# Optimization experiments

Measured on AMD Instinct MI355X. Metric: run time of the kernel, lower is better.

Reference implementation:

```python
import jax, jax.numpy as jnp
import numpy as np

D_MODEL = 512
HEADS = 8
FF_HIDDEN = 1024
EPS = 1e-6


def setup_inputs() -> dict:
    key = jax.random.key(0)
    ks = jax.random.split(key, 12)
    s = 1.0 / np.sqrt(D_MODEL)
    inp = {
        'x': jax.random.normal(ks[0], (2, 4096, D_MODEL), dtype=jnp.float32),
        'Wq': jax.random.normal(ks[1], (D_MODEL, D_MODEL), dtype=jnp.float32) * s,
        'bq': jnp.zeros((D_MODEL,), jnp.float32),
        'Wk': jax.random.normal(ks[2], (D_MODEL, D_MODEL), dtype=jnp.float32) * s,
        'bk': jnp.zeros((D_MODEL,), jnp.float32),
        'Wv': jax.random.normal(ks[3], (D_MODEL, D_MODEL), dtype=jnp.float32) * s,
        'bv': jnp.zeros((D_MODEL,), jnp.float32),
        'Wo': jax.random.normal(ks[4], (D_MODEL, D_MODEL), dtype=jnp.float32) * s,
        'bo': jnp.zeros((D_MODEL,), jnp.float32),
        'a1': jnp.ones((D_MODEL,), jnp.float32),
        'b1': jnp.zeros((D_MODEL,), jnp.float32),
        'a2': jnp.ones((D_MODEL,), jnp.float32),
        'b2': jnp.zeros((D_MODEL,), jnp.float32),
        'W1': jax.random.normal(ks[5], (D_MODEL, FF_HIDDEN), dtype=jnp.float32) * s,
        'c1': jnp.zeros((FF_HIDDEN,), jnp.float32),
        'W2': jax.random.normal(ks[6], (FF_HIDDEN, D_MODEL), dtype=jnp.float32) * (1.0 / np.sqrt(FF_HIDDEN)),
        'c2': jnp.zeros((D_MODEL,), jnp.float32),
    }
    return inp


def _layer_norm(x, a, b):
    # Faithful to source: uses unbiased std (torch default) and divides by (std + eps)
    mean = jnp.mean(x, axis=-1, keepdims=True)
    std = jnp.std(x, axis=-1, keepdims=True, ddof=1)
    return a * ((x - mean) / (std + EPS)) + b


def _encoder_block(x, Wq, bq, Wk, bk, Wv, bv, Wo, bo, a1, b1, a2, b2, W1, c1, W2, c2):
    B, S, D = x.shape
    H, dk = HEADS, D // HEADS
    q = (x @ Wq + bq).reshape(B, S, H, dk).transpose(0, 2, 1, 3)  # [B,H,S,dk]
    k = (x @ Wk + bk).reshape(B, S, H, dk).transpose(0, 2, 1, 3)
    v = (x @ Wv + bv).reshape(B, S, H, dk).transpose(0, 2, 1, 3)
    scores = jnp.einsum('bhqd,bhkd->bhqk', q, k) / np.sqrt(dk)
    probs = jax.nn.softmax(scores, axis=-1)
    attn = jnp.einsum('bhqk,bhkd->bhqd', probs, v)
    concat = attn.transpose(0, 2, 1, 3).reshape(B, S, D)
    attn_out = concat @ Wo + bo
    x = _layer_norm(x + attn_out, a1, b1)  # dropout = identity (eval mode)
    ffn = jax.nn.relu(x @ W1 + c1) @ W2 + c2
    return _layer_norm(x + ffn, a2, b2)


def reference(x, Wq, bq, Wk, bk, Wv, bv, Wo, bo, a1, b1, a2, b2, W1, c1, W2, c2):
    return _encoder_block(x, Wq, bq, Wk, bk, Wv, bv, Wo, bo, a1, b1, a2, b2, W1, c1, W2, c2)
```

## Files before the change

kernel.cpp:

```cpp
#include <hip/hip_runtime.h>
#include <stdint.h>

typedef short short8 __attribute__((ext_vector_type(8)));
typedef float f32x4 __attribute__((ext_vector_type(4)));
typedef float f32x16 __attribute__((ext_vector_type(16)));
typedef unsigned int u32x4 __attribute__((ext_vector_type(4)));

#define LOG2E 1.44269504088896f

__device__ __forceinline__ unsigned short f2b(float f) {
  union { float f; unsigned int u; } x; x.f = f;
  unsigned int u = x.u;
  unsigned int r = (u + 0x7fffu + ((u >> 16) & 1u)) >> 16;
  return (unsigned short)r;
}
__device__ __forceinline__ float b2f(unsigned short s) {
  union { unsigned int u; float f; } x; x.u = ((unsigned int)s) << 16;
  return x.f;
}
__device__ __forceinline__ void gl16(const void* g, void* l) {
  __builtin_amdgcn_global_load_lds((const __attribute__((address_space(1))) void*)g,
                                   (__attribute__((address_space(3))) void*)l, 16, 0, 0);
}
__device__ __forceinline__ unsigned int cvtpk(float lo, float hi) {
  unsigned int r;
  asm("v_cvt_pk_bf16_f32 %0, %1, %2" : "=v"(r) : "v"(lo), "v"(hi));
  return r;
}
__device__ __forceinline__ void plswap(unsigned int& a, unsigned int& b) {
  asm volatile("v_permlane32_swap_b32 %0, %1" : "+v"(a), "+v"(b));
}

__global__ __launch_bounds__(256) void castx_k(const float* __restrict__ X,
                                               unsigned short* __restrict__ Xb) {
  int i = blockIdx.x * 256 + threadIdx.x;
  const float* p = X + (size_t)i * 8;
  float4 a = *(const float4*)(p);
  float4 b = *(const float4*)(p + 4);
  short8 o;
  o[0] = (short)f2b(a.x); o[1] = (short)f2b(a.y);
  o[2] = (short)f2b(a.z); o[3] = (short)f2b(a.w);
  o[4] = (short)f2b(b.x); o[5] = (short)f2b(b.y);
  o[6] = (short)f2b(b.z); o[7] = (short)f2b(b.w);
  *(short8*)(Xb + (size_t)i * 8) = o;
}

__global__ __launch_bounds__(256) void catb_k(const float* __restrict__ bq,
                                              const float* __restrict__ bk,
                                              const float* __restrict__ bv,
                                              float* __restrict__ Bqkv) {
  for (int i = threadIdx.x; i < 1536; i += 256) {
    float v = (i < 512) ? bq[i] : (i < 1024 ? bk[i - 512] : bv[i - 1024]);
    Bqkv[i] = v;
  }
}

__global__ __launch_bounds__(256) void wtrans_k(const float* __restrict__ W,
                                                unsigned short* __restrict__ WT,
                                                int K, int N) {
  __shared__ float t[64][65];
  int k0 = blockIdx.x * 64, n0 = blockIdx.y * 64;
  for (int i = threadIdx.x; i < 4096; i += 256) {
    int r = i >> 6, c = i & 63;
    t[r][c] = W[(size_t)(k0 + r) * N + n0 + c];
  }
  __syncthreads();
  for (int i = threadIdx.x; i < 4096; i += 256) {
    int r = i >> 6, c = i & 63;
    WT[(size_t)(n0 + r) * K + k0 + c] = f2b(t[c][r]);
  }
}

__global__ __launch_bounds__(256) void vtrans_k(const unsigned short* __restrict__ V,
                                                unsigned short* __restrict__ Vt) {
  __shared__ unsigned short t[64][65];
  int s0 = blockIdx.x * 64;
  int bh = blockIdx.y;
  int b = bh >> 3, h = bh & 7;
  for (int i = threadIdx.x; i < 4096; i += 256) {
    int r = i >> 6, c = i & 63;
    t[r][c] = V[(size_t)(b * 4096 + s0 + r) * 512 + h * 64 + c];
  }
  __syncthreads();
  for (int i = threadIdx.x; i < 4096; i += 256) {
    int r = i >> 6, c = i & 63;
    Vt[(size_t)(bh * 64 + r) * 4096 + s0 + c] = t[c][r];
  }
}

template <int EPI>
__global__ __launch_bounds__(256) void gemm_bt(
    const unsigned short* __restrict__ A, const unsigned short* __restrict__ BT,
    const float* __restrict__ bias, float* __restrict__ Cf,
    unsigned short* __restrict__ Cb, int M, int N, int K) {
  __shared__ unsigned short As[128 * 32];
  __shared__ unsigned short Bs[128 * 32];
  int t = threadIdx.x, w = t >> 6, l = t & 63;
  int bm = blockIdx.x, bn = blockIdx.y;
  int wm = w >> 1, wn = w & 1;
  int g = l >> 4, ln = l & 15;
  f32x4 acc[4][4] = {};
  const unsigned short* Arow = A + (size_t)bm * 128 * K;
  const unsigned short* Brow = BT + (size_t)bn * 128 * K;
  int nk = K >> 5;
  for (int kt = 0; kt < nk; ++kt) {
    int k0 = kt * 32;
#pragma unroll
    for (int i = 0; i < 2; ++i) {
      int cl = i * 256 + t;
      int r = cl >> 2, c = cl & 3;
      char* ldsA = (char*)As + (size_t)(i * 256 + w * 64) * 16;
      char* ldsB = (char*)Bs + (size_t)(i * 256 + w * 64) * 16;
      gl16(Arow + (size_t)r * K + k0 + c * 8, ldsA);
      gl16(Brow + (size_t)r * K + k0 + c * 8, ldsB);
    }
    __syncthreads();
    short8 af[4], bf[4];
    int ko = g * 8;
#pragma unroll
    for (int i = 0; i < 4; ++i)
      af[i] = *(const short8*)&As[(wm * 64 + i * 16 + ln) * 32 + ko];
#pragma unroll
    for (int j = 0; j < 4; ++j)
      bf[j] = *(const short8*)&Bs[(wn * 64 + j * 16 + ln) * 32 + ko];
    __builtin_amdgcn_s_setprio(1);
#pragma unroll
    for (int i = 0; i < 4; ++i)
#pragma unroll
      for (int j = 0; j < 4; ++j)
        acc[i][j] = __builtin_amdgcn_mfma_f32_16x16x32_bf16(af[i], bf[j], acc[i][j], 0, 0, 0);
    __builtin_amdgcn_s_setprio(0);
    __syncthreads();
  }
#pragma unroll
  for (int i = 0; i < 4; ++i) {
    int row = bm * 128 + wm * 64 + i * 16 + g * 4;
#pragma unroll
    for (int j = 0; j < 4; ++j) {
      int col = bn * 128 + wn * 64 + j * 16 + ln;
      float bv = bias[col];
#pragma unroll
      for (int r = 0; r < 4; ++r) {
        float v = acc[i][j][r] + bv;
        if constexpr (EPI == 2) v = v > 0.f ? v : 0.f;
        if constexpr (EPI == 0) Cf[(size_t)(row + r) * N + col] = v;
        else if constexpr (EPI == 3)
          Cb[(size_t)(col >> 9) * 4194304 + (size_t)(row + r) * 512 + (col & 511)] = f2b(v);
        else Cb[(size_t)(row + r) * N + col] = f2b(v);
      }
    }
  }
}

__global__ __launch_bounds__(256) void gemm64_k(
    const unsigned short* __restrict__ A, const unsigned short* __restrict__ BT,
    const float* __restrict__ bias, float* __restrict__ Cf, int M, int N, int K) {
  __shared__ unsigned short As[64 * 32];
  __shared__ unsigned short Bs[128 * 32];
  int t = threadIdx.x, w = t >> 6, l = t & 63;
  int bm = blockIdx.x, bn = blockIdx.y;
  int wm = w >> 1, wn = w & 1;
  int g = l >> 4, ln = l & 15;
  f32x4 acc[2][4] = {};
  const unsigned short* Arow = A + (size_t)bm * 64 * K;
  const unsigned short* Brow = BT + (size_t)bn * 128 * K;
  int nk = K >> 5;
  for (int kt = 0; kt < nk; ++kt) {
    int k0 = kt * 32;
    {
      int r = t >> 2, c = t & 3;
      gl16(Arow + (size_t)r * K + k0 + c * 8, (char*)As + (size_t)(w * 64) * 16);
    }
#pragma unroll
    for (int i = 0; i < 2; ++i) {
      int cl = i * 256 + t;
      int r = cl >> 2, c = cl & 3;
      char* ldsB = (char*)Bs + (size_t)(i * 256 + w * 64) * 16;
      gl16(Brow + (size_t)r * K + k0 + c * 8, ldsB);
    }
    __syncthreads();
    short8 af[2], bf[4];
    int ko = g * 8;
#pragma unroll
    for (int i = 0; i < 2; ++i)
      af[i] = *(const short8*)&As[(wm * 32 + i * 16 + ln) * 32 + ko];
#pragma unroll
    for (int j = 0; j < 4; ++j)
      bf[j] = *(const short8*)&Bs[(wn * 64 + j * 16 + ln) * 32 + ko];
    __builtin_amdgcn_s_setprio(1);
#pragma unroll
    for (int i = 0; i < 2; ++i)
#pragma unroll
      for (int j = 0; j < 4; ++j)
        acc[i][j] = __builtin_amdgcn_mfma_f32_16x16x32_bf16(af[i], bf[j], acc[i][j], 0, 0, 0);
    __builtin_amdgcn_s_setprio(0);
    __syncthreads();
  }
#pragma unroll
  for (int i = 0; i < 2; ++i) {
    int row = bm * 64 + wm * 32 + i * 16 + g * 4;
#pragma unroll
    for (int j = 0; j < 4; ++j) {
      int col = bn * 128 + wn * 64 + j * 16 + ln;
      float bv = bias[col];
#pragma unroll
      for (int r = 0; r < 4; ++r)
        Cf[(size_t)(row + r) * N + col] = acc[i][j][r] + bv;
    }
  }
}

__global__ __launch_bounds__(256, 2) void attn_k(
    const unsigned short* __restrict__ Q, const unsigned short* __restrict__ Kb,
    const unsigned short* __restrict__ Vt, float* __restrict__ Opart,
    float* __restrict__ L) {
  __shared__ unsigned short Ks[2][4096];
  __shared__ unsigned short Vs[3][4096];
  int tid = threadIdx.x, wv = tid >> 6, lane = tid & 63;
  int l31 = lane & 31, hi = lane >> 5;
  int qb = blockIdx.x, bh = blockIdx.y, z = blockIdx.z;
  int b = bh >> 3, h = bh & 7;
  int q0 = qb * 256 + wv * 64;
  int kvbase = z * 2048;

  short8 qfA[4], qfB[4];
  {
    const float QSC = 0.125f * LOG2E;
    const unsigned short* qpA = Q + (size_t)(b * 4096 + q0 + l31) * 512 + h * 64;
    const unsigned short* qpB = qpA + 32 * 512;
#pragma unroll
    for (int ks = 0; ks < 4; ++ks) {
      short8 va = *(const short8*)(qpA + ks * 16 + hi * 8);
      short8 vb = *(const short8*)(qpB + ks * 16 + hi * 8);
#pragma unroll
      for (int j = 0; j < 8; ++j) {
        va[j] = (short)f2b(b2f((unsigned short)va[j]) * QSC);
        vb[j] = (short)f2b(b2f((unsigned short)vb[j]) * QSC);
      }
      qfA[ks] = va; qfB[ks] = vb;
    }
  }

  short8 ones;
#pragma unroll
  for (int j = 0; j < 8; ++j) ones[j] = (short)0x3F80;

  f32x16 oA0 = {}, oA1 = {}, oB0 = {}, oB1 = {}, laccA = {}, laccB = {};

  int skk[2], sc[2];
#pragma unroll
  for (int i = 0; i < 2; ++i) {
    int u = i * 256 + tid;
    int r2 = u >> 4, s = u & 15;
    skk[i] = 2 * r2 + (s & 1);
    sc[i] = ((s >> 1) ^ (r2 & 7)) * 8;
  }

  auto stage = [&](char* kb_lds, char* vb_lds, int kv) {
    const unsigned short* ksrc = Kb + (size_t)(b * 4096 + kv) * 512 + h * 64;
    const unsigned short* vsrc = Vt + (size_t)(bh * 64) * 4096 + kv;
#pragma unroll
    for (int i = 0; i < 2; ++i) {
      gl16(ksrc + (size_t)skk[i] * 512 + sc[i], kb_lds + (size_t)(i * 256 + wv * 64) * 16);
      gl16(vsrc + (size_t)skk[i] * 4096 + sc[i], vb_lds + (size_t)(i * 256 + wv * 64) * 16);
    }
  };

  int r2a = l31 >> 1, par = l31 & 1, perm = r2a & 7;
  int rdb = r2a * 256 + (par << 4);

  auto qk = [&](const char* kbase, f32x16& sA0, f32x16& sA1, f32x16& sB0, f32x16& sB1) {
    __builtin_amdgcn_s_setprio(1);
#pragma unroll
    for (int ks = 0; ks < 4; ++ks) {
      int c16 = ks * 2 + hi;
      int byteA = rdb + (((c16 ^ perm) << 1) << 4);
      short8 k0 = *(const short8*)(kbase + byteA);
      short8 k1 = *(const short8*)(kbase + byteA + 4096);
      sA0 = __builtin_amdgcn_mfma_f32_32x32x16_bf16(k0, qfA[ks], sA0, 0, 0, 0);
      sA1 = __builtin_amdgcn_mfma_f32_32x32x16_bf16(k1, qfA[ks], sA1, 0, 0, 0);
      sB0 = __builtin_amdgcn_mfma_f32_32x32x16_bf16(k0, qfB[ks], sB0, 0, 0, 0);
      sB1 = __builtin_amdgcn_mfma_f32_32x32x16_bf16(k1, qfB[ks], sB1, 0, 0, 0);
    }
    __builtin_amdgcn_s_setprio(0);
  };

  auto pv = [&](const char* vbase, const short8* pfA, const short8* pfB) {
    __builtin_amdgcn_s_setprio(1);
#pragma unroll
    for (int ks = 0; ks < 4; ++ks) {
      int c16 = ks * 2 + hi;
      int byteA = rdb + (((c16 ^ perm) << 1) << 4);
      short8 v0 = *(const short8*)(vbase + byteA);
      short8 v1 = *(const short8*)(vbase + byteA + 4096);
      oA0 = __builtin_amdgcn_mfma_f32_32x32x16_bf16(v0, pfA[ks], oA0, 0, 0, 0);
      oA1 = __builtin_amdgcn_mfma_f32_32x32x16_bf16(v1, pfA[ks], oA1, 0, 0, 0);
      oB0 = __builtin_amdgcn_mfma_f32_32x32x16_bf16(v0, pfB[ks], oB0, 0, 0, 0);
      oB1 = __builtin_amdgcn_mfma_f32_32x32x16_bf16(v1, pfB[ks], oB1, 0, 0, 0);
      laccA = __builtin_amdgcn_mfma_f32_32x32x16_bf16(ones, pfA[ks], laccA, 0, 0, 0);
      laccB = __builtin_amdgcn_mfma_f32_32x32x16_bf16(ones, pfB[ks], laccB, 0, 0, 0);
    }
    __builtin_amdgcn_s_setprio(0);
  };

  auto exppack = [&](f32x16& s0, f32x16& s1, short8* pf) {
#pragma unroll
    for (int r = 0; r < 16; ++r) s0[r] = __builtin_amdgcn_exp2f(s0[r]);
#pragma unroll
    for (int r = 0; r < 16; ++r) s1[r] = __builtin_amdgcn_exp2f(s1[r]);
    unsigned int u0 = cvtpk(s0[0], s0[1]), u1 = cvtpk(s0[4], s0[5]);
    plswap(u0, u1);
    unsigned int u2 = cvtpk(s0[2], s0[3]), u3 = cvtpk(s0[6], s0[7]);
    plswap(u2, u3);
    unsigned int u4 = cvtpk(s0[8], s0[9]), u5 = cvtpk(s0[12], s0[13]);
    plswap(u4, u5);
    unsigned int u6 = cvtpk(s0[10], s0[11]), u7 = cvtpk(s0[14], s0[15]);
    plswap(u6, u7);
    union { u32x4 u; short8 s; } cv;
    cv.u = (u32x4){u0, u2, u1, u3}; pf[0] = cv.s;
    cv.u = (u32x4){u4, u6, u5, u7}; pf[1] = cv.s;
    unsigned int w0 = cvtpk(s1[0], s1[1]), w1 = cvtpk(s1[4], s1[5]);
    plswap(w0, w1);
    unsigned int w2 = cvtpk(s1[2], s1[3]), w3 = cvtpk(s1[6], s1[7]);
    plswap(w2, w3);
    unsigned int w4 = cvtpk(s1[8], s1[9]), w5 = cvtpk(s1[12], s1[13]);
    plswap(w4, w5);
    unsigned int w6 = cvtpk(s1[10], s1[11]), w7 = cvtpk(s1[14], s1[15]);
    plswap(w6, w7);
    cv.u = (u32x4){w0, w2, w1, w3}; pf[2] = cv.s;
    cv.u = (u32x4){w4, w6, w5, w7}; pf[3] = cv.s;
  };

  char* k0b = (char*)&Ks[0][0];
  char* k1b = (char*)&Ks[1][0];
  char* vA = (char*)&Vs[0][0];
  char* vB = (char*)&Vs[1][0];
  char* vC = (char*)&Vs[2][0];
  stage(k0b, vA, kvbase);
  __syncthreads();
  stage(k1b, vB, kvbase + 64);

  f32x16 sA0 = {}, sA1 = {}, sB0 = {}, sB1 = {};
  qk(k0b, sA0, sA1, sB0, sB1);
  short8 pfA[4], pfB[4];
  exppack(sA0, sA1, pfA);
  exppack(sB0, sB1, pfB);

#pragma unroll 1
  for (int t = 1; t < 32; ++t) {
    __syncthreads();
    char* kr = (t & 1) ? k1b : k0b;
    char* kw = (t & 1) ? k0b : k1b;
    if (t < 31) stage(kw, vC, kvbase + (t + 1) * 64);
    sA0 = (f32x16){}; sA1 = (f32x16){}; sB0 = (f32x16){}; sB1 = (f32x16){};
    qk(kr, sA0, sA1, sB0, sB1);
    pv(vA, pfA, pfB);
    exppack(sA0, sA1, pfA);
    exppack(sB0, sB1, pfB);
    char* tmp = vA; vA = vB; vB = vC; vC = tmp;
  }
  pv(vA, pfA, pfB);

  int plane = z * 16 + bh;
  float* op = Opart + (size_t)plane * 262144;
  int qA = q0 + l31, qB = q0 + 32 + l31;
#pragma unroll
  for (int r = 0; r < 16; ++r) {
    int dr = (r & 3) + 8 * (r >> 2) + 4 * hi;
    op[(size_t)dr * 4096 + qA] = oA0[r];
    op[(size_t)(dr + 32) * 4096 + qA] = oA1[r];
    op[(size_t)dr * 4096 + qB] = oB0[r];
    op[(size_t)(dr + 32) * 4096 + qB] = oB1[r];
  }
  if (hi == 0) {
    L[(size_t)plane * 4096 + qA] = laccA[0];
    L[(size_t)plane * 4096 + qB] = laccB[0];
  }
}

__global__ __launch_bounds__(256) void comb_k(const float* __restrict__ Opart,
                                              const float* __restrict__ L,
                                              unsigned short* __restrict__ O) {
  __shared__ float sli[64];
  __shared__ unsigned short tt[64][80];
  int tid = threadIdx.x;
  int qt = blockIdx.x, bh = blockIdx.y;
  int b = bh >> 3, h = bh & 7;
  int q0 = qt * 64;
  if (tid < 64) {
    int q = q0 + tid;
    sli[tid] = 1.0f / (L[(size_t)bh * 4096 + q] + L[(size_t)(16 + bh) * 4096 + q]);
  }
  __syncthreads();
  const float* p0 = Opart + (size_t)bh * 262144;
  const float* p1 = Opart + (size_t)(16 + bh) * 262144;
  int d = tid >> 2, qg = tid & 3;
#pragma unroll
  for (int i = 0; i < 16; ++i) {
    int qq = qg * 16 + i;
    size_t idx = (size_t)d * 4096 + q0 + qq;
    tt[qq][d] = f2b((p0[idx] + p1[idx]) * sli[qq]);
  }
  __syncthreads();
  int qr = tid >> 2, dc = tid & 3;
  short8 v0 = *(const short8*)&tt[qr][dc * 16];
  short8 v1 = *(const short8*)&tt[qr][dc * 16 + 8];
  size_t row = (size_t)(b * 4096 + q0 + qr);
  *(short8*)(O + row * 512 + h * 64 + dc * 16) = v0;
  *(short8*)(O + row * 512 + h * 64 + dc * 16 + 8) = v1;
}

template <bool WB>
__global__ __launch_bounds__(256) void ln_k(const float* __restrict__ X,
                                            const float* __restrict__ Y,
                                            const float* __restrict__ gamma,
                                            const float* __restrict__ beta,
                                            float* __restrict__ outf,
                                            unsigned short* __restrict__ outb) {
  int w = threadIdx.x >> 6, l = threadIdx.x & 63;
  size_t row = (size_t)blockIdx.x * 4 + w;
  const float* xr = X + row * 512;
  const float* yr = Y + row * 512;
  float vals[8];
  float s = 0.f, ss = 0.f;
#pragma unroll
  for (int i = 0; i < 2; ++i) {
    float4 a = *(const float4*)(xr + l * 8 + i * 4);
    float4 c = *(const float4*)(yr + l * 8 + i * 4);
    vals[i * 4 + 0] = a.x + c.x; vals[i * 4 + 1] = a.y + c.y;
    vals[i * 4 + 2] = a.z + c.z; vals[i * 4 + 3] = a.w + c.w;
  }
#pragma unroll
  for (int j = 0; j < 8; ++j) { s += vals[j]; ss += vals[j] * vals[j]; }
#pragma unroll
  for (int off = 1; off < 64; off <<= 1) { s += __shfl_xor(s, off); ss += __shfl_xor(ss, off); }
  float mean = s * (1.f / 512.f);
  float var = fmaxf((ss - 512.f * mean * mean) * (1.f / 511.f), 0.f);
  float inv = 1.f / (sqrtf(var) + 1e-6f);
  unsigned short bvals[8];
#pragma unroll
  for (int i = 0; i < 2; ++i) {
    float4 gm = *(const float4*)(gamma + l * 8 + i * 4);
    float4 bt = *(const float4*)(beta + l * 8 + i * 4);
    float4 o;
    o.x = gm.x * ((vals[i * 4 + 0] - mean) * inv) + bt.x;
    o.y = gm.y * ((vals[i * 4 + 1] - mean) * inv) + bt.y;
    o.z = gm.z * ((vals[i * 4 + 2] - mean) * inv) + bt.z;
    o.w = gm.w * ((vals[i * 4 + 3] - mean) * inv) + bt.w;
    *(float4*)(outf + row * 512 + l * 8 + i * 4) = o;
    if constexpr (WB) {
      bvals[i * 4 + 0] = f2b(o.x); bvals[i * 4 + 1] = f2b(o.y);
      bvals[i * 4 + 2] = f2b(o.z); bvals[i * 4 + 3] = f2b(o.w);
    }
  }
  if constexpr (WB) {
    short8 pk;
#pragma unroll
    for (int j = 0; j < 8; ++j) pk[j] = (short)bvals[j];
    *(short8*)(outb + row * 512 + l * 8) = pk;
  }
}

extern "C" void kernel_launch(void* const* d_in, const int* in_sizes, int n_in,
                              void* d_out, int out_size, void* d_ws, size_t ws_size,
                              hipStream_t stream) {
  const float* x  = (const float*)d_in[0];
  const float* Wq = (const float*)d_in[1];
  const float* bq = (const float*)d_in[2];
  const float* Wk = (const float*)d_in[3];
  const float* bk = (const float*)d_in[4];
  const float* Wv = (const float*)d_in[5];
  const float* bv = (const float*)d_in[6];
  const float* Wo = (const float*)d_in[7];
  const float* bo = (const float*)d_in[8];
  const float* a1 = (const float*)d_in[9];
  const float* b1 = (const float*)d_in[10];
  const float* a2 = (const float*)d_in[11];
  const float* b2 = (const float*)d_in[12];
  const float* W1 = (const float*)d_in[13];
  const float* c1 = (const float*)d_in[14];
  const float* W2 = (const float*)d_in[15];
  const float* c2 = (const float*)d_in[16];

  char* ws = (char*)d_ws;
  const size_t MB = 1024 * 1024;
  unsigned short* Xb  = (unsigned short*)(ws + 0);
  unsigned short* Qb  = (unsigned short*)(ws + 8 * MB);
  unsigned short* Kbf = (unsigned short*)(ws + 16 * MB);
  unsigned short* Vb  = (unsigned short*)(ws + 24 * MB);
  unsigned short* Vtb = (unsigned short*)(ws + 32 * MB);
  unsigned short* WqkvT = (unsigned short*)(ws + 40 * MB);
  unsigned short* WoT = (unsigned short*)(ws + 41 * MB + 512 * 1024);
  unsigned short* W1T = (unsigned short*)(ws + 42 * MB);
  unsigned short* W2T = (unsigned short*)(ws + 43 * MB);
  float* AO = (float*)(ws + 44 * MB);
  float* Y1 = (float*)(ws + 60 * MB);
  unsigned short* Att = Xb;
  unsigned short* Y1b = Qb;
  unsigned short* Hb  = Kbf;
  float* Opart = AO;
  float* L = (float*)(ws + 24 * MB);
  float* Bqkv = Y1;

  castx_k<<<2048, 256, 0, stream>>>(x, Xb);
  catb_k<<<1, 256, 0, stream>>>(bq, bk, bv, Bqkv);
  wtrans_k<<<dim3(8, 8), 256, 0, stream>>>(Wq, WqkvT, 512, 512);
  wtrans_k<<<dim3(8, 8), 256, 0, stream>>>(Wk, WqkvT + 512 * 512, 512, 512);
  wtrans_k<<<dim3(8, 8), 256, 0, stream>>>(Wv, WqkvT + 2 * 512 * 512, 512, 512);
  wtrans_k<<<dim3(8, 8), 256, 0, stream>>>(Wo, WoT, 512, 512);
  wtrans_k<<<dim3(8, 16), 256, 0, stream>>>(W1, W1T, 512, 1024);
  wtrans_k<<<dim3(16, 8), 256, 0, stream>>>(W2, W2T, 1024, 512);

  gemm_bt<3><<<dim3(64, 12), 256, 0, stream>>>(Xb, WqkvT, Bqkv, nullptr, Qb, 8192, 1536, 512);

  vtrans_k<<<dim3(64, 16), 256, 0, stream>>>(Vb, Vtb);
  attn_k<<<dim3(16, 16, 2), 256, 0, stream>>>(Qb, Kbf, Vtb, Opart, L);
  comb_k<<<dim3(64, 16), 256, 0, stream>>>(Opart, L, Att);

  gemm64_k<<<dim3(128, 4), 256, 0, stream>>>(Att, WoT, bo, AO, 8192, 512, 512);
  ln_k<true><<<2048, 256, 0, stream>>>(x, AO, a1, b1, Y1, Y1b);
  gemm_bt<2><<<dim3(64, 8), 256, 0, stream>>>(Y1b, W1T, c1, nullptr, Hb, 8192, 1024, 512);
  gemm64_k<<<dim3(128, 4), 256, 0, stream>>>(Hb, W2T, c2, AO, 8192, 512, 1024);
  ln_k<false><<<2048, 256, 0, stream>>>(Y1, AO, a2, b2, (float*)d_out, nullptr);
}
```

Baseline: 227.8 us.

## Fuse LayerNorm into GEMMs, write V transposed from QKV GEMM, fold Q scale

Several changes at once. The Wo and W2 GEMMs become a 16-row-by-512-column kernel that adds the residual and applies LayerNorm in its epilogue, which removes the fp32 AO round-trip and the separate ln_k launches. The QKV GEMM writes V straight into the transposed layout, so vtrans_k goes away, and the Q softmax scale is folded into Wq and bq. Attention partial outputs are stored as bf16 instead of fp32, and the first QK MFMA takes a zero accumulator. Risks: the new GEMM tile is narrow in M and reloads the whole B matrix per block, the bf16 partials lose precision, and the transposed V writes are strided.

```diff
diff --git a/kernel.cpp b/kernel.cpp
--- a/kernel.cpp
+++ b/kernel.cpp
@@ -2,11 +2,13 @@
 #include <stdint.h>
 
 typedef short short8 __attribute__((ext_vector_type(8)));
+typedef short short4v __attribute__((ext_vector_type(4)));
 typedef float f32x4 __attribute__((ext_vector_type(4)));
 typedef float f32x16 __attribute__((ext_vector_type(16)));
 typedef unsigned int u32x4 __attribute__((ext_vector_type(4)));
 
 #define LOG2E 1.44269504088896f
+#define QSCALE (0.125f * LOG2E)
 
 __device__ __forceinline__ unsigned short f2b(float f) {
   union { float f; unsigned int u; } x; x.f = f;
@@ -50,14 +52,14 @@
                                               const float* __restrict__ bv,
                                               float* __restrict__ Bqkv) {
   for (int i = threadIdx.x; i < 1536; i += 256) {
-    float v = (i < 512) ? bq[i] : (i < 1024 ? bk[i - 512] : bv[i - 1024]);
+    float v = (i < 512) ? bq[i] * QSCALE : (i < 1024 ? bk[i - 512] : bv[i - 1024]);
     Bqkv[i] = v;
   }
 }
 
 __global__ __launch_bounds__(256) void wtrans_k(const float* __restrict__ W,
                                                 unsigned short* __restrict__ WT,
-                                                int K, int N) {
+                                                int K, int N, float scale) {
   __shared__ float t[64][65];
   int k0 = blockIdx.x * 64, n0 = blockIdx.y * 64;
   for (int i = threadIdx.x; i < 4096; i += 256) {
@@ -67,24 +69,7 @@
   __syncthreads();
   for (int i = threadIdx.x; i < 4096; i += 256) {
     int r = i >> 6, c = i & 63;
-    WT[(size_t)(n0 + r) * K + k0 + c] = f2b(t[c][r]);
-  }
-}
-
-__global__ __launch_bounds__(256) void vtrans_k(const unsigned short* __restrict__ V,
-                                                unsigned short* __restrict__ Vt) {
-  __shared__ unsigned short t[64][65];
-  int s0 = blockIdx.x * 64;
-  int bh = blockIdx.y;
-  int b = bh >> 3, h = bh & 7;
-  for (int i = threadIdx.x; i < 4096; i += 256) {
-    int r = i >> 6, c = i & 63;
-    t[r][c] = V[(size_t)(b * 4096 + s0 + r) * 512 + h * 64 + c];
-  }
-  __syncthreads();
-  for (int i = threadIdx.x; i < 4096; i += 256) {
-    int r = i >> 6, c = i & 63;
-    Vt[(size_t)(bh * 64 + r) * 4096 + s0 + c] = t[c][r];
+    WT[(size_t)(n0 + r) * K + k0 + c] = f2b(t[c][r] * scale);
   }
 }
 
@@ -139,80 +124,130 @@
     for (int j = 0; j < 4; ++j) {
       int col = bn * 128 + wn * 64 + j * 16 + ln;
       float bv = bias[col];
+      float vv[4];
 #pragma unroll
       for (int r = 0; r < 4; ++r) {
         float v = acc[i][j][r] + bv;
         if constexpr (EPI == 2) v = v > 0.f ? v : 0.f;
-        if constexpr (EPI == 0) Cf[(size_t)(row + r) * N + col] = v;
-        else if constexpr (EPI == 3)
-          Cb[(size_t)(col >> 9) * 4194304 + (size_t)(row + r) * 512 + (col & 511)] = f2b(v);
-        else Cb[(size_t)(row + r) * N + col] = f2b(v);
+        vv[r] = v;
       }
-    }
-  }
-}
-
-__global__ __launch_bounds__(256) void gemm64_k(
+      if constexpr (EPI == 3) {
+        if (col < 1024) {
+#pragma unroll
+          for (int r = 0; r < 4; ++r)
+            Cb[(size_t)(col >> 9) * 4194304 + (size_t)(row + r) * 512 + (col & 511)] = f2b(vv[r]);
+        } else {
+          short4v pk;
+#pragma unroll
+          for (int r = 0; r < 4; ++r) pk[r] = (short)f2b(vv[r]);
+          *(short4v*)((unsigned short*)Cf +
+                      (size_t)((row >> 12) * 512 + (col & 511)) * 4096 + (row & 4095)) = pk;
+        }
+      } else {
+#pragma unroll
+        for (int r = 0; r < 4; ++r)
+          Cb[(size_t)(row + r) * N + col] = f2b(vv[r]);
+      }
+    }
+  }
+}
+
+template <bool WB>
+__global__ __launch_bounds__(512) void gemmln_k(
     const unsigned short* __restrict__ A, const unsigned short* __restrict__ BT,
-    const float* __restrict__ bias, float* __restrict__ Cf, int M, int N, int K) {
-  __shared__ unsigned short As[64 * 32];
-  __shared__ unsigned short Bs[128 * 32];
-  int t = threadIdx.x, w = t >> 6, l = t & 63;
-  int bm = blockIdx.x, bn = blockIdx.y;
-  int wm = w >> 1, wn = w & 1;
-  int g = l >> 4, ln = l & 15;
-  f32x4 acc[2][4] = {};
-  const unsigned short* Arow = A + (size_t)bm * 64 * K;
-  const unsigned short* Brow = BT + (size_t)bn * 128 * K;
+    const float* __restrict__ bias, const float* __restrict__ X,
+    const float* __restrict__ gamma, const float* __restrict__ beta,
+    float* __restrict__ outf, unsigned short* __restrict__ outb, int K) {
+  __shared__ unsigned short As[16 * 32];
+  __shared__ unsigned short Bs[512 * 32];
+  __shared__ float stats[8][16][2];
+  __shared__ float minv[16][2];
+  int tid = threadIdx.x, wv = tid >> 6, lane = tid & 63;
+  int g = lane >> 4, ln = lane & 15;
+  int bm = blockIdx.x;
+  f32x4 acc[4] = {};
+  const unsigned short* Arow = A + (size_t)bm * 16 * K;
   int nk = K >> 5;
   for (int kt = 0; kt < nk; ++kt) {
     int k0 = kt * 32;
-    {
-      int r = t >> 2, c = t & 3;
-      gl16(Arow + (size_t)r * K + k0 + c * 8, (char*)As + (size_t)(w * 64) * 16);
-    }
-#pragma unroll
-    for (int i = 0; i < 2; ++i) {
-      int cl = i * 256 + t;
-      int r = cl >> 2, c = cl & 3;
-      char* ldsB = (char*)Bs + (size_t)(i * 256 + w * 64) * 16;
-      gl16(Brow + (size_t)r * K + k0 + c * 8, ldsB);
+    if (tid < 64) {
+      int r = tid >> 2, c = tid & 3;
+      gl16(Arow + (size_t)r * K + k0 + c * 8, (char*)As + tid * 16);
+    }
+#pragma unroll
+    for (int i = 0; i < 4; ++i) {
+      int u = i * 512 + tid;
+      int r = u >> 2, c = u & 3;
+      gl16(BT + (size_t)r * K + k0 + c * 8, (char*)Bs + (size_t)u * 16);
     }
     __syncthreads();
-    short8 af[2], bf[4];
-    int ko = g * 8;
-#pragma unroll
-    for (int i = 0; i < 2; ++i)
-      af[i] = *(const short8*)&As[(wm * 32 + i * 16 + ln) * 32 + ko];
-#pragma unroll
-    for (int j = 0; j < 4; ++j)
-      bf[j] = *(const short8*)&Bs[(wn * 64 + j * 16 + ln) * 32 + ko];
+    short8 af = *(const short8*)&As[ln * 32 + g * 8];
     __builtin_amdgcn_s_setprio(1);
 #pragma unroll
-    for (int i = 0; i < 2; ++i)
-#pragma unroll
-      for (int j = 0; j < 4; ++j)
-        acc[i][j] = __builtin_amdgcn_mfma_f32_16x16x32_bf16(af[i], bf[j], acc[i][j], 0, 0, 0);
+    for (int j = 0; j < 4; ++j) {
+      short8 bf = *(const short8*)&Bs[(wv * 64 + j * 16 + ln) * 32 + g * 8];
+      acc[j] = __builtin_amdgcn_mfma_f32_16x16x32_bf16(af, bf, acc[j], 0, 0, 0);
+    }
     __builtin_amdgcn_s_setprio(0);
     __syncthreads();
   }
-#pragma unroll
-  for (int i = 0; i < 2; ++i) {
-    int row = bm * 64 + wm * 32 + i * 16 + g * 4;
-#pragma unroll
-    for (int j = 0; j < 4; ++j) {
-      int col = bn * 128 + wn * 64 + j * 16 + ln;
-      float bv = bias[col];
-#pragma unroll
-      for (int r = 0; r < 4; ++r)
-        Cf[(size_t)(row + r) * N + col] = acc[i][j][r] + bv;
+  int row0 = bm * 16;
+  float v[4][4];
+  float ps[4] = {0.f, 0.f, 0.f, 0.f}, pss[4] = {0.f, 0.f, 0.f, 0.f};
+#pragma unroll
+  for (int j = 0; j < 4; ++j) {
+    int col = wv * 64 + j * 16 + ln;
+    float bv = bias[col];
+#pragma unroll
+    for (int r = 0; r < 4; ++r) {
+      float t = acc[j][r] + bv + X[(size_t)(row0 + g * 4 + r) * 512 + col];
+      v[j][r] = t;
+      ps[r] += t; pss[r] += t * t;
+    }
+  }
+#pragma unroll
+  for (int off = 1; off < 16; off <<= 1) {
+#pragma unroll
+    for (int r = 0; r < 4; ++r) {
+      ps[r] += __shfl_xor(ps[r], off);
+      pss[r] += __shfl_xor(pss[r], off);
+    }
+  }
+  if (ln == 0) {
+#pragma unroll
+    for (int r = 0; r < 4; ++r) {
+      stats[wv][g * 4 + r][0] = ps[r];
+      stats[wv][g * 4 + r][1] = pss[r];
+    }
+  }
+  __syncthreads();
+  if (tid < 16) {
+    float S = 0.f, SS = 0.f;
+#pragma unroll
+    for (int w2 = 0; w2 < 8; ++w2) { S += stats[w2][tid][0]; SS += stats[w2][tid][1]; }
+    float mean = S * (1.f / 512.f);
+    float var = fmaxf((SS - 512.f * mean * mean) * (1.f / 511.f), 0.f);
+    minv[tid][0] = mean;
+    minv[tid][1] = 1.f / (sqrtf(var) + 1e-6f);
+  }
+  __syncthreads();
+#pragma unroll
+  for (int j = 0; j < 4; ++j) {
+    int col = wv * 64 + j * 16 + ln;
+    float gm = gamma[col], bt2 = beta[col];
+#pragma unroll
+    for (int r = 0; r < 4; ++r) {
+      int row = g * 4 + r;
+      float o = gm * ((v[j][r] - minv[row][0]) * minv[row][1]) + bt2;
+      outf[(size_t)(row0 + row) * 512 + col] = o;
+      if constexpr (WB) outb[(size_t)(row0 + row) * 512 + col] = f2b(o);
     }
   }
 }
 
 __global__ __launch_bounds__(256, 2) void attn_k(
     const unsigned short* __restrict__ Q, const unsigned short* __restrict__ Kb,
-    const unsigned short* __restrict__ Vt, float* __restrict__ Opart,
+    const unsigned short* __restrict__ Vt, unsigned short* __restrict__ Opart,
     float* __restrict__ L) {
   __shared__ unsigned short Ks[2][4096];
   __shared__ unsigned short Vs[3][4096];
@@ -225,19 +260,12 @@
 
   short8 qfA[4], qfB[4];
   {
-    const float QSC = 0.125f * LOG2E;
     const unsigned short* qpA = Q + (size_t)(b * 4096 + q0 + l31) * 512 + h * 64;
     const unsigned short* qpB = qpA + 32 * 512;
 #pragma unroll
     for (int ks = 0; ks < 4; ++ks) {
-      short8 va = *(const short8*)(qpA + ks * 16 + hi * 8);
-      short8 vb = *(const short8*)(qpB + ks * 16 + hi * 8);
-#pragma unroll
-      for (int j = 0; j < 8; ++j) {
-        va[j] = (short)f2b(b2f((unsigned short)va[j]) * QSC);
-        vb[j] = (short)f2b(b2f((unsigned short)vb[j]) * QSC);
-      }
-      qfA[ks] = va; qfB[ks] = vb;
+      qfA[ks] = *(const short8*)(qpA + ks * 16 + hi * 8);
+      qfB[ks] = *(const short8*)(qpB + ks * 16 + hi * 8);
     }
   }
 
@@ -245,6 +273,7 @@
 #pragma unroll
   for (int j = 0; j < 8; ++j) ones[j] = (short)0x3F80;
 
+  const f32x16 Z = {};
   f32x16 oA0 = {}, oA1 = {}, oB0 = {}, oB1 = {}, laccA = {}, laccB = {};
 
   int skk[2], sc[2];
@@ -277,10 +306,17 @@
       int byteA = rdb + (((c16 ^ perm) << 1) << 4);
       short8 k0 = *(const short8*)(kbase + byteA);
       short8 k1 = *(const short8*)(kbase + byteA + 4096);
-      sA0 = __builtin_amdgcn_mfma_f32_32x32x16_bf16(k0, qfA[ks], sA0, 0, 0, 0);
-      sA1 = __builtin_amdgcn_mfma_f32_32x32x16_bf16(k1, qfA[ks], sA1, 0, 0, 0);
-      sB0 = __builtin_amdgcn_mfma_f32_32x32x16_bf16(k0, qfB[ks], sB0, 0, 0, 0);
-      sB1 = __builtin_amdgcn_mfma_f32_32x32x16_bf16(k1, qfB[ks], sB1, 0, 0, 0);
+      if (ks == 0) {
+        sA0 = __builtin_amdgcn_mfma_f32_32x32x16_bf16(k0, qfA[0], Z, 0, 0, 0);
+        sA1 = __builtin_amdgcn_mfma_f32_32x32x16_bf16(k1, qfA[0], Z, 0, 0, 0);
+        sB0 = __builtin_amdgcn_mfma_f32_32x32x16_bf16(k0, qfB[0], Z, 0, 0, 0);
+        sB1 = __builtin_amdgcn_mfma_f32_32x32x16_bf16(k1, qfB[0], Z, 0, 0, 0);
+      } else {
+        sA0 = __builtin_amdgcn_mfma_f32_32x32x16_bf16(k0, qfA[ks], sA0, 0, 0, 0);
+        sA1 = __builtin_amdgcn_mfma_f32_32x32x16_bf16(k1, qfA[ks], sA1, 0, 0, 0);
+        sB0 = __builtin_amdgcn_mfma_f32_32x32x16_bf16(k0, qfB[ks], sB0, 0, 0, 0);
+        sB1 = __builtin_amdgcn_mfma_f32_32x32x16_bf16(k1, qfB[ks], sB1, 0, 0, 0);
+      }
     }
     __builtin_amdgcn_s_setprio(0);
   };
@@ -340,7 +376,7 @@
   __syncthreads();
   stage(k1b, vB, kvbase + 64);
 
-  f32x16 sA0 = {}, sA1 = {}, sB0 = {}, sB1 = {};
+  f32x16 sA0, sA1, sB0, sB1;
   qk(k0b, sA0, sA1, sB0, sB1);
   short8 pfA[4], pfB[4];
   exppack(sA0, sA1, pfA);
@@ -352,7 +388,6 @@
     char* kr = (t & 1) ? k1b : k0b;
     char* kw = (t & 1) ? k0b : k1b;
     if (t < 31) stage(kw, vC, kvbase + (t + 1) * 64);
-    sA0 = (f32x16){}; sA1 = (f32x16){}; sB0 = (f32x16){}; sB1 = (f32x16){};
     qk(kr, sA0, sA1, sB0, sB1);
     pv(vA, pfA, pfB);
     exppack(sA0, sA1, pfA);
@@ -362,15 +397,15 @@
   pv(vA, pfA, pfB);
 
   int plane = z * 16 + bh;
-  float* op = Opart + (size_t)plane * 262144;
+  unsigned short* op = Opart + (size_t)plane * 262144;
   int qA = q0 + l31, qB = q0 + 32 + l31;
 #pragma unroll
   for (int r = 0; r < 16; ++r) {
     int dr = (r & 3) + 8 * (r >> 2) + 4 * hi;
-    op[(size_t)dr * 4096 + qA] = oA0[r];
-    op[(size_t)(dr + 32) * 4096 + qA] = oA1[r];
-    op[(size_t)dr * 4096 + qB] = oB0[r];
-    op[(size_t)(dr + 32) * 4096 + qB] = oB1[r];
+    op[(size_t)dr * 4096 + qA] = f2b(oA0[r]);
+    op[(size_t)(dr + 32) * 4096 + qA] = f2b(oA1[r]);
+    op[(size_t)dr * 4096 + qB] = f2b(oB0[r]);
+    op[(size_t)(dr + 32) * 4096 + qB] = f2b(oB1[r]);
   }
   if (hi == 0) {
     L[(size_t)plane * 4096 + qA] = laccA[0];
@@ -378,7 +413,7 @@
   }
 }
 
-__global__ __launch_bounds__(256) void comb_k(const float* __restrict__ Opart,
+__global__ __launch_bounds__(256) void comb_k(const unsigned short* __restrict__ Opart,
                                               const float* __restrict__ L,
                                               unsigned short* __restrict__ O) {
   __shared__ float sli[64];
@@ -392,14 +427,14 @@
     sli[tid] = 1.0f / (L[(size_t)bh * 4096 + q] + L[(size_t)(16 + bh) * 4096 + q]);
   }
   __syncthreads();
-  const float* p0 = Opart + (size_t)bh * 262144;
-  const float* p1 = Opart + (size_t)(16 + bh) * 262144;
+  const unsigned short* p0 = Opart + (size_t)bh * 262144;
+  const unsigned short* p1 = Opart + (size_t)(16 + bh) * 262144;
   int d = tid >> 2, qg = tid & 3;
 #pragma unroll
   for (int i = 0; i < 16; ++i) {
     int qq = qg * 16 + i;
     size_t idx = (size_t)d * 4096 + q0 + qq;
-    tt[qq][d] = f2b((p0[idx] + p1[idx]) * sli[qq]);
+    tt[qq][d] = f2b((b2f(p0[idx]) + b2f(p1[idx])) * sli[qq]);
   }
   __syncthreads();
   int qr = tid >> 2, dc = tid & 3;
@@ -408,57 +443,6 @@
   size_t row = (size_t)(b * 4096 + q0 + qr);
   *(short8*)(O + row * 512 + h * 64 + dc * 16) = v0;
   *(short8*)(O + row * 512 + h * 64 + dc * 16 + 8) = v1;
-}
-
-template <bool WB>
-__global__ __launch_bounds__(256) void ln_k(const float* __restrict__ X,
-                                            const float* __restrict__ Y,
-                                            const float* __restrict__ gamma,
-                                            const float* __restrict__ beta,
-                                            float* __restrict__ outf,
-                                            unsigned short* __restrict__ outb) {
-  int w = threadIdx.x >> 6, l = threadIdx.x & 63;
-  size_t row = (size_t)blockIdx.x * 4 + w;
-  const float* xr = X + row * 512;
-  const float* yr = Y + row * 512;
-  float vals[8];
-  float s = 0.f, ss = 0.f;
-#pragma unroll
-  for (int i = 0; i < 2; ++i) {
-    float4 a = *(const float4*)(xr + l * 8 + i * 4);
-    float4 c = *(const float4*)(yr + l * 8 + i * 4);
-    vals[i * 4 + 0] = a.x + c.x; vals[i * 4 + 1] = a.y + c.y;
-    vals[i * 4 + 2] = a.z + c.z; vals[i * 4 + 3] = a.w + c.w;
-  }
-#pragma unroll
-  for (int j = 0; j < 8; ++j) { s += vals[j]; ss += vals[j] * vals[j]; }
-#pragma unroll
-  for (int off = 1; off < 64; off <<= 1) { s += __shfl_xor(s, off); ss += __shfl_xor(ss, off); }
-  float mean = s * (1.f / 512.f);
-  float var = fmaxf((ss - 512.f * mean * mean) * (1.f / 511.f), 0.f);
-  float inv = 1.f / (sqrtf(var) + 1e-6f);
-  unsigned short bvals[8];
-#pragma unroll
-  for (int i = 0; i < 2; ++i) {
-    float4 gm = *(const float4*)(gamma + l * 8 + i * 4);
-    float4 bt = *(const float4*)(beta + l * 8 + i * 4);
-    float4 o;
-    o.x = gm.x * ((vals[i * 4 + 0] - mean) * inv) + bt.x;
-    o.y = gm.y * ((vals[i * 4 + 1] - mean) * inv) + bt.y;
-    o.z = gm.z * ((vals[i * 4 + 2] - mean) * inv) + bt.z;
-    o.w = gm.w * ((vals[i * 4 + 3] - mean) * inv) + bt.w;
-    *(float4*)(outf + row * 512 + l * 8 + i * 4) = o;
-    if constexpr (WB) {
-      bvals[i * 4 + 0] = f2b(o.x); bvals[i * 4 + 1] = f2b(o.y);
-      bvals[i * 4 + 2] = f2b(o.z); bvals[i * 4 + 3] = f2b(o.w);
-    }
-  }
-  if constexpr (WB) {
-    short8 pk;
-#pragma unroll
-    for (int j = 0; j < 8; ++j) pk[j] = (short)bvals[j];
-    *(short8*)(outb + row * 512 + l * 8) = pk;
-  }
 }
 
 extern "C" void kernel_launch(void* const* d_in, const int* in_sizes, int n_in,
@@ -487,39 +471,34 @@
   unsigned short* Xb  = (unsigned short*)(ws + 0);
   unsigned short* Qb  = (unsigned short*)(ws + 8 * MB);
   unsigned short* Kbf = (unsigned short*)(ws + 16 * MB);
-  unsigned short* Vb  = (unsigned short*)(ws + 24 * MB);
+  float* L = (float*)(ws + 24 * MB);
   unsigned short* Vtb = (unsigned short*)(ws + 32 * MB);
   unsigned short* WqkvT = (unsigned short*)(ws + 40 * MB);
   unsigned short* WoT = (unsigned short*)(ws + 41 * MB + 512 * 1024);
   unsigned short* W1T = (unsigned short*)(ws + 42 * MB);
   unsigned short* W2T = (unsigned short*)(ws + 43 * MB);
-  float* AO = (float*)(ws + 44 * MB);
+  unsigned short* Opart = (unsigned short*)(ws + 44 * MB);
+  float* Bqkv = (float*)(ws + 44 * MB);
   float* Y1 = (float*)(ws + 60 * MB);
   unsigned short* Att = Xb;
   unsigned short* Y1b = Qb;
   unsigned short* Hb  = Kbf;
-  float* Opart = AO;
-  float* L = (float*)(ws + 24 * MB);
-  float* Bqkv = Y1;
 
   castx_k<<<2048, 256, 0, stream>>>(x, Xb);
   catb_k<<<1, 256, 0, stream>>>(bq, bk, bv, Bqkv);
-  wtrans_k<<<dim3(8, 8), 256, 0, stream>>>(Wq, WqkvT, 512, 512);
-  wtrans_k<<<dim3(8, 8), 256, 0, stream>>>(Wk, WqkvT + 512 * 512, 512, 512);
-  wtrans_k<<<dim3(8, 8), 256, 0, stream>>>(Wv, WqkvT + 2 * 512 * 512, 512, 512);
-  wtrans_k<<<dim3(8, 8), 256, 0, stream>>>(Wo, WoT, 512, 512);
-  wtrans_k<<<dim3(8, 16), 256, 0, stream>>>(W1, W1T, 512, 1024);
-  wtrans_k<<<dim3(16, 8), 256, 0, stream>>>(W2, W2T, 1024, 512);
-
-  gemm_bt<3><<<dim3(64, 12), 256, 0, stream>>>(Xb, WqkvT, Bqkv, nullptr, Qb, 8192, 1536, 512);
-
-  vtrans_k<<<dim3(64, 16), 256, 0, stream>>>(Vb, Vtb);
+  wtrans_k<<<dim3(8, 8), 256, 0, stream>>>(Wq, WqkvT, 512, 512, QSCALE);
+  wtrans_k<<<dim3(8, 8), 256, 0, stream>>>(Wk, WqkvT + 512 * 512, 512, 512, 1.0f);
+  wtrans_k<<<dim3(8, 8), 256, 0, stream>>>(Wv, WqkvT + 2 * 512 * 512, 512, 512, 1.0f);
+  wtrans_k<<<dim3(8, 8), 256, 0, stream>>>(Wo, WoT, 512, 512, 1.0f);
+  wtrans_k<<<dim3(8, 16), 256, 0, stream>>>(W1, W1T, 512, 1024, 1.0f);
+  wtrans_k<<<dim3(16, 8), 256, 0, stream>>>(W2, W2T, 1024, 512, 1.0f);
+
+  gemm_bt<3><<<dim3(64, 12), 256, 0, stream>>>(Xb, WqkvT, Bqkv, (float*)Vtb, Qb, 8192, 1536, 512);
+
   attn_k<<<dim3(16, 16, 2), 256, 0, stream>>>(Qb, Kbf, Vtb, Opart, L);
   comb_k<<<dim3(64, 16), 256, 0, stream>>>(Opart, L, Att);
 
-  gemm64_k<<<dim3(128, 4), 256, 0, stream>>>(Att, WoT, bo, AO, 8192, 512, 512);
-  ln_k<true><<<2048, 256, 0, stream>>>(x, AO, a1, b1, Y1, Y1b);
+  gemmln_k<true><<<512, 512, 0, stream>>>(Att, WoT, bo, x, a1, b1, Y1, Y1b, 512);
   gemm_bt<2><<<dim3(64, 8), 256, 0, stream>>>(Y1b, W1T, c1, nullptr, Hb, 8192, 1024, 512);
-  gemm64_k<<<dim3(128, 4), 256, 0, stream>>>(Hb, W2T, c2, AO, 8192, 512, 1024);
-  ln_k<false><<<2048, 256, 0, stream>>>(Y1, AO, a2, b2, (float*)d_out, nullptr);
-}
+  gemmln_k<false><<<512, 512, 0, stream>>>(Hb, W2T, c2, Y1, a2, b2, (float*)d_out, nullptr, 1024);
+}
```

Measured after the change: 222.6 us. 2.3% less time.
